# Performance work log

Hardware: AMD Instinct MI355X
Metric: run time of the kernel (lower is better)

The kernel has to match this reference:

```python
import jax, jax.numpy as jnp
import numpy as np

B, N, X, Y, W1, W2, D = 2, 6, 8, 8, 8, 8, 128
H, DH = 4, 32
L = X * Y          # number of windows
QT = N * W1 * W2   # tokens per window
EPS = 1e-5


def _ln(x, g, b):
    m = x.mean(-1, keepdims=True)
    v = ((x - m) ** 2).mean(-1, keepdims=True)
    return (x - m) * jax.lax.rsqrt(v + EPS) * g + b


def _win(t):
    # b n x y w1 w2 d -> b (x y) (n w1 w2) d
    return t.transpose(0, 2, 3, 1, 4, 5, 6).reshape(B, L, QT, D)


def setup_inputs() -> dict:
    key = jax.random.key(0)
    ks = jax.random.split(key, 12)
    s = 0.02
    inp = {
        'q': jax.random.normal(ks[0], (B, N, X, Y, W1, W2, D), jnp.float32),
        'k': jax.random.normal(ks[1], (B, N, X, Y, W1, W2, D), jnp.float32),
        'v': jax.random.normal(ks[2], (B, N, X, Y, W1, W2, D), jnp.float32),
        'skip': jax.random.normal(ks[3], (B, X, Y, W1, W2, D), jnp.float32),
        'gq': jnp.ones((D,), jnp.float32), 'betq': jnp.zeros((D,), jnp.float32),
        'gk': jnp.ones((D,), jnp.float32), 'betk': jnp.zeros((D,), jnp.float32),
        'gv': jnp.ones((D,), jnp.float32), 'betv': jnp.zeros((D,), jnp.float32),
        'wq': jax.random.normal(ks[4], (D, H * DH), jnp.float32) * s,
        'bq': jnp.zeros((H * DH,), jnp.float32),
        'wk': jax.random.normal(ks[5], (D, H * DH), jnp.float32) * s,
        'bk': jnp.zeros((H * DH,), jnp.float32),
        'wv': jax.random.normal(ks[6], (D, H * DH), jnp.float32) * s,
        'bv': jnp.zeros((H * DH,), jnp.float32),
        'wp': jax.random.normal(ks[7], (H * DH, D), jnp.float32) * s,
        'bp': jnp.zeros((D,), jnp.float32),
    }
    return inp


def reference(q, k, v, skip, gq, betq, gk, betk, gv, betv,
              wq, bq, wk, bk, wv, bv, wp, bp):
    scale = DH ** -0.5
    qw, kw, vw = _win(q), _win(k), _win(v)
    # LayerNorm + Linear QKV, split heads: (b, l, T, h, dh)
    qh = (_ln(qw, gq, betq) @ wq + bq).reshape(B, L, QT, H, DH)
    kh = (_ln(kw, gk, betk) @ wk + bk).reshape(B, L, QT, H, DH)
    vh = (_ln(vw, gv, betv) @ wv + bv).reshape(B, L, QT, H, DH)
    dot = scale * jnp.einsum('blqhd,blkhd->bhlqk', qh, kh)
    att = jax.nn.softmax(dot, axis=-1)
    a = jnp.einsum('bhlqk,blkhd->blqhd', att, vh).reshape(B, L, QT, H * DH)
    # b (x y) (n w1 w2) d -> b n x y w1 w2 d
    a = a.reshape(B, X, Y, N, W1, W2, H * DH).transpose(0, 3, 1, 2, 4, 5, 6)
    z = a @ wp + bp
    z = z.mean(1)  # average over views
    return z + skip
```

## Files before the change

### kernel.cpp

```cpp
#include <hip/hip_runtime.h>


typedef unsigned short u16;
typedef __bf16 bf16x8 __attribute__((ext_vector_type(8)));
typedef __bf16 bf16x4 __attribute__((ext_vector_type(4)));
typedef float  f32x16 __attribute__((ext_vector_type(16)));
typedef unsigned short u16x8 __attribute__((ext_vector_type(8)));

union U8 { u16x8 u; bf16x8 b; };

#if __has_builtin(__builtin_amdgcn_exp2f)
#define EXP2(x) __builtin_amdgcn_exp2f(x)
#else
#define EXP2(x) exp2f(x)
#endif

__device__ __forceinline__ f32x16 mfma_bf16(bf16x8 a, bf16x8 b, f32x16 c){
  return __builtin_amdgcn_mfma_f32_32x32x16_bf16(a, b, c, 0, 0, 0);
}


__global__ __launch_bounds__(512) void k_prep(
    const float* __restrict__ wq, const float* __restrict__ bq,
    const float* __restrict__ gq, const float* __restrict__ betq,
    const float* __restrict__ wk, const float* __restrict__ bk,
    const float* __restrict__ gk, const float* __restrict__ betk,
    const float* __restrict__ wv, const float* __restrict__ bv,
    const float* __restrict__ gv, const float* __restrict__ betv,
    const float* __restrict__ wp,
    u16* __restrict__ wqT, u16* __restrict__ wkT, u16* __restrict__ wvT, u16* __restrict__ wpT,
    float* __restrict__ bq2, float* __restrict__ bk2, float* __restrict__ bv2,
    float* __restrict__ uq2, float* __restrict__ uk2, float* __restrict__ uv2)
{
  __shared__ float wls[128*129];
  __shared__ float gls[128], bls[128];
  __shared__ float redb[512], redu[512];
  const float ALPHA_Q = 0.17677669529663687f * 1.4426950408889634f;
  int wsel = blockIdx.x, tid = threadIdx.x;
  const float *w, *bb, *g, *bet; u16* wT; float *b2, *u2; float alpha;
  if (wsel == 0){ w=wq; bb=bq; g=gq; bet=betq; wT=wqT; b2=bq2; u2=uq2; alpha=ALPHA_Q; }
  else if (wsel == 1){ w=wk; bb=bk; g=gk; bet=betk; wT=wkT; b2=bk2; u2=uk2; alpha=1.f; }
  else if (wsel == 2){ w=wv; bb=bv; g=gv; bet=betv; wT=wvT; b2=bv2; u2=uv2; alpha=1.f; }
  else { w=wp; bb=nullptr; g=nullptr; bet=nullptr; wT=wpT; b2=nullptr; u2=nullptr; alpha=1.f; }

  if (tid < 128){
    gls[tid] = g ? g[tid] : 1.f;
    bls[tid] = bet ? bet[tid] : 0.f;
  }
  const float4* w4 = (const float4*)w;
  #pragma unroll
  for (int i = 0; i < 8; i++){
    int idx = tid + i*512;
    int row = idx >> 5, c4 = (idx & 31) * 4;
    float4 x = w4[idx];
    wls[row*129 + c4 + 0] = x.x;
    wls[row*129 + c4 + 1] = x.y;
    wls[row*129 + c4 + 2] = x.z;
    wls[row*129 + c4 + 3] = x.w;
  }
  __syncthreads();
  int n = tid >> 2, qp = tid & 3;
  float sb = 0.f, su = 0.f;
  alignas(16) __bf16 tmp[32];
  #pragma unroll
  for (int kk = 0; kk < 32; kk++){
    int k2 = qp*32 + kk;
    float wv_ = wls[k2*129 + n];
    float gv_ = gls[k2];
    sb += bls[k2] * wv_;
    su += gv_ * wv_;
    tmp[kk] = (__bf16)(wv_ * gv_ * alpha);
  }
  #pragma unroll
  for (int j = 0; j < 4; j++)
    *(bf16x8*)(wT + n*128 + qp*32 + j*8) = *(bf16x8*)&tmp[j*8];
  redb[tid] = sb; redu[tid] = su;
  __syncthreads();
  if (qp == 0 && bb){
    float s = bb[n] + redb[tid] + redb[tid+1] + redb[tid+2] + redb[tid+3];
    float u = redu[tid] + redu[tid+1] + redu[tid+2] + redu[tid+3];
    b2[n] = s * alpha;
    u2[n] = u * alpha;
  }
}

__global__ __launch_bounds__(256) void k_lnproj(
    const float* __restrict__ qg, const float* __restrict__ kg, const float* __restrict__ vg,
    const u16* __restrict__ wqT, const u16* __restrict__ wkT, const u16* __restrict__ wvT,
    const float* __restrict__ bq2, const float* __restrict__ bk2, const float* __restrict__ bv2,
    const float* __restrict__ uq2, const float* __restrict__ uk2, const float* __restrict__ uv2,
    u16* __restrict__ qh, u16* __restrict__ kh, u16* __restrict__ vh)
{
  __shared__ alignas(16) u16 Abf[64*136];
  __shared__ float s1s[64], s2s[64];
  int bid = blockIdx.x, tid = threadIdx.x;
  int which = bid % 3;
  int t = bid / 3;
  int n = t % 6, bl = t / 6;
  const float* src; const u16* wT; const float *b2, *u2; u16* dstb;
  if (which == 0){ src=qg; wT=wqT; b2=bq2; u2=uq2; dstb=qh; }
  else if (which == 1){ src=kg; wT=wkT; b2=bk2; u2=uk2; dstb=kh; }
  else { src=vg; wT=wvT; b2=bv2; u2=uv2; dstb=vh; }
  int b = bl >> 6, l = bl & 63;
  const float4* s4 = (const float4*)(src + (size_t)((b*6 + n)*64 + l)*64*128);
  int row = tid >> 2, j = tid & 3;
  float s1 = 0.f, s2 = 0.f;
  #pragma unroll
  for (int i = 0; i < 8; i++){
    float4 xv = s4[row*32 + i*4 + j];
    s1 += xv.x + xv.y + xv.z + xv.w;
    s2 += xv.x*xv.x + xv.y*xv.y + xv.z*xv.z + xv.w*xv.w;
    bf16x4 pk;
    pk[0] = (__bf16)xv.x; pk[1] = (__bf16)xv.y;
    pk[2] = (__bf16)xv.z; pk[3] = (__bf16)xv.w;
    *(bf16x4*)&Abf[row*136 + (i*4 + j)*4] = pk;
  }
  s1 += __shfl_xor(s1, 1, 64); s1 += __shfl_xor(s1, 2, 64);
  s2 += __shfl_xor(s2, 1, 64); s2 += __shfl_xor(s2, 2, 64);
  if (j == 0){
    float m = s1 * (1.f/128.f);
    float r = rsqrtf(s2 * (1.f/128.f) - m*m + 1e-5f);
    s1s[row] = r;
    s2s[row] = r * m;
  }
  __syncthreads();
  int wave = tid >> 6, lane = tid & 63, lm = lane & 31, lh = lane >> 5;
  bf16x8 bfr[8];
  const u16* wrow = wT + (32*wave + lm)*128 + lh*8;
  #pragma unroll
  for (int ks = 0; ks < 8; ks++) bfr[ks] = *(const bf16x8*)(wrow + ks*16);
  f32x16 acc0, acc1;
  #pragma unroll
  for (int r = 0; r < 16; r++){ acc0[r]=0.f; acc1[r]=0.f; }
  #pragma unroll
  for (int ks = 0; ks < 8; ks++){
    bf16x8 a0 = *(const bf16x8*)&Abf[lm*136       + ks*16 + lh*8];
    bf16x8 a1 = *(const bf16x8*)&Abf[(32+lm)*136  + ks*16 + lh*8];
    acc0 = mfma_bf16(a0, bfr[ks], acc0);
    acc1 = mfma_bf16(a1, bfr[ks], acc1);
  }
  int col = 32*wave + lm;
  float u2c = u2[col], bc = b2[col];
  u16* dst = dstb + ((size_t)(bl*4 + wave)*384 + n*64)*32 + lm;
  #pragma unroll
  for (int r = 0; r < 16; r++){
    int row0 = (r&3) + 8*(r>>2) + 4*lh;
    float y0 = s1s[row0]     * acc0[r] - s2s[row0]     * u2c + bc;
    float y1 = s1s[row0+32]  * acc1[r] - s2s[row0+32]  * u2c + bc;
    *(__bf16*)&dst[(size_t)row0*32]      = (__bf16)y0;
    *(__bf16*)&dst[(size_t)(32+row0)*32] = (__bf16)y1;
  }
}

__global__ __launch_bounds__(768, 6) void k_attn(
    const u16* __restrict__ qh, const u16* __restrict__ kh, const u16* __restrict__ vh,
    u16* __restrict__ abar)
{
  __shared__ alignas(16) u16 vts[32*408];
  __shared__ float abar_s[64*32];
  int bid = blockIdx.x, tid = threadIdx.x;
  int h = bid & 3, bl = bid >> 2;
  const u16* qb = qh + (size_t)bid * (384*32);
  const u16* kb = kh + (size_t)bid * (384*32);
  const u16* vb = vh + (size_t)bid * (384*32);

  int wave = tid >> 6, lane = tid & 63, lm = lane & 31, lh = lane >> 5;
  int n = wave >> 1, qoff = (wave & 1) * 32;
  int qrow = n*64 + qoff + lm;

  bf16x8 qf0 = *(const bf16x8*)(qb + qrow*32 +      lh*8);
  bf16x8 qf1 = *(const bf16x8*)(qb + qrow*32 + 16 + lh*8);
  bf16x8 kf0[2], kf1[2];
  kf0[0] = *(const bf16x8*)(kb + lm*32 +      lh*8);
  kf1[0] = *(const bf16x8*)(kb + lm*32 + 16 + lh*8);

  #pragma unroll
  for (int i = 0; i < 2; i++){
    int c = tid + i*768;
    int key = c >> 2, part = c & 3;
    int u = key & 31, tt = key >> 5;
    int a = u >> 2;
    int anew = (a & 4) | ((a & 1) << 1) | ((a >> 1) & 1);
    int pos = tt*32 + anew*4 + (u & 3);
    u16x8 vv = *(const u16x8*)(vb + key*32 + part*8);
    #pragma unroll
    for (int jj = 0; jj < 8; jj++) vts[(part*8 + jj)*408 + pos] = vv[jj];
  }
  for (int idx = tid; idx < 2048; idx += 768) abar_s[idx] = 0.f;
  __syncthreads();

  const u16* vrow = &vts[lm*408 + 8*lh];
  U8 v0[2], v1[2];
  v0[0].u = *(const u16x8*)(vrow);
  v1[0].u = *(const u16x8*)(vrow + 16);

  f32x16 oacc;
  #pragma unroll
  for (int r = 0; r < 16; r++) oacc[r] = 0.f;
  float sle = 0.f;

  #pragma unroll
  for (int kt = 0; kt < 12; kt++){
    int cur = kt & 1, nxt = cur ^ 1;
    if (kt < 11){
      int K1 = (kt+1)*32;
      kf0[nxt] = *(const bf16x8*)(kb + (K1+lm)*32 +      lh*8);
      kf1[nxt] = *(const bf16x8*)(kb + (K1+lm)*32 + 16 + lh*8);
      v0[nxt].u = *(const u16x8*)(vrow + K1);
      v1[nxt].u = *(const u16x8*)(vrow + K1 + 16);
    }
    f32x16 s;
    #pragma unroll
    for (int r = 0; r < 16; r++) s[r] = 0.f;
    s = mfma_bf16(kf0[cur], qf0, s);
    s = mfma_bf16(kf1[cur], qf1, s);
    U8 p0, p1;
    #pragma unroll
    for (int r = 0; r < 8; r++){
      float e0 = EXP2(s[r]);
      float e1 = EXP2(s[r+8]);
      sle += e0 + e1;
      p0.b[r] = (__bf16)e0;
      p1.b[r] = (__bf16)e1;
    }
    oacc = mfma_bf16(p0.b, v0[cur].b, oacc);
    oacc = mfma_bf16(p1.b, v1[cur].b, oacc);
  }

  sle += __shfl_xor(sle, 32, 64);
  float inv = (1.f/6.f) / sle;

  #pragma unroll
  for (int r = 0; r < 16; r++){
    int q_l = (r&3) + 8*(r>>2) + 4*lh;
    float o = oacc[r] * __shfl(inv, q_l, 64);
    atomicAdd(&abar_s[(qoff + q_l)*32 + lm], o);
  }
  __syncthreads();
  u16* ob = abar + (size_t)(bl*64)*128 + h*32;
  for (int idx = tid; idx < 2048; idx += 768){
    int w12 = idx >> 5, dh = idx & 31;
    *(__bf16*)&ob[(size_t)w12*128 + dh] = (__bf16)abar_s[idx];
  }
}

__global__ __launch_bounds__(256) void k_out(
    const u16* __restrict__ abar, const u16* __restrict__ wpT,
    const float* __restrict__ bp, const float* __restrict__ skip,
    float* __restrict__ out)
{
  __shared__ alignas(16) u16 Als[64*136];
  int tid = threadIdx.x;
  int R0 = blockIdx.x * 64;
  #pragma unroll
  for (int i = 0; i < 4; i++){
    int c = tid + i*256;
    int row = c >> 4, part = c & 15;
    *(u16x8*)&Als[row*136 + part*8] = *(const u16x8*)(abar + (size_t)(R0+row)*128 + part*8);
  }
  __syncthreads();
  int wave = tid >> 6, lane = tid & 63, lm = lane & 31, lh = lane >> 5;
  bf16x8 bfr[8];
  const u16* wrow = wpT + (32*wave + lm)*128 + lh*8;
  #pragma unroll
  for (int ks = 0; ks < 8; ks++) bfr[ks] = *(const bf16x8*)(wrow + ks*16);
  f32x16 acc0, acc1;
  #pragma unroll
  for (int r = 0; r < 16; r++){ acc0[r]=0.f; acc1[r]=0.f; }
  #pragma unroll
  for (int ks = 0; ks < 8; ks++){
    bf16x8 a0 = *(const bf16x8*)&Als[lm*136      + ks*16 + lh*8];
    bf16x8 a1 = *(const bf16x8*)&Als[(32+lm)*136 + ks*16 + lh*8];
    acc0 = mfma_bf16(a0, bfr[ks], acc0);
    acc1 = mfma_bf16(a1, bfr[ks], acc1);
  }
  float bias = bp[32*wave + lm];
  #pragma unroll
  for (int r = 0; r < 16; r++){
    int row0 = (r&3) + 8*(r>>2) + 4*lh;
    size_t f0 = (size_t)(R0 + row0)*128 + 32*wave + lm;
    out[f0] = acc0[r] + bias + skip[f0];
    size_t f1 = (size_t)(R0 + 32 + row0)*128 + 32*wave + lm;
    out[f1] = acc1[r] + bias + skip[f1];
  }
}

extern "C" void kernel_launch(void* const* d_in, const int* in_sizes, int n_in,
                              void* d_out, int out_size, void* d_ws, size_t ws_size,
                              hipStream_t stream)
{
  const float* q    = (const float*)d_in[0];
  const float* k    = (const float*)d_in[1];
  const float* v    = (const float*)d_in[2];
  const float* skip = (const float*)d_in[3];
  const float* gq   = (const float*)d_in[4];
  const float* betq = (const float*)d_in[5];
  const float* gk   = (const float*)d_in[6];
  const float* betk = (const float*)d_in[7];
  const float* gv   = (const float*)d_in[8];
  const float* betv = (const float*)d_in[9];
  const float* wq   = (const float*)d_in[10];
  const float* bq   = (const float*)d_in[11];
  const float* wk   = (const float*)d_in[12];
  const float* bk   = (const float*)d_in[13];
  const float* wv   = (const float*)d_in[14];
  const float* bv   = (const float*)d_in[15];
  const float* wp   = (const float*)d_in[16];
  const float* bp   = (const float*)d_in[17];
  float* out = (float*)d_out;

  char* ws = (char*)d_ws;
  u16* wqT = (u16*)ws;
  u16* wkT = wqT + 16384;
  u16* wvT = wkT + 16384;
  u16* wpT = wvT + 16384;
  float* bq2 = (float*)(ws + 131072);
  float* bk2 = bq2 + 128;
  float* bv2 = bk2 + 128;
  float* uq2 = bv2 + 128;
  float* uk2 = uq2 + 128;
  float* uv2 = uk2 + 128;
  u16* qh = (u16*)(ws + 134144);
  u16* kh = qh + 6291456;
  u16* vh = kh + 6291456;
  u16* abar = vh + 6291456;

  k_prep  <<<4,    512, 0, stream>>>(wq,bq,gq,betq, wk,bk,gk,betk, wv,bv,gv,betv, wp,
                                     wqT,wkT,wvT,wpT, bq2,bk2,bv2, uq2,uk2,uv2);
  k_lnproj<<<2304, 256, 0, stream>>>(q,k,v, wqT,wkT,wvT, bq2,bk2,bv2, uq2,uk2,uv2, qh,kh,vh);
  k_attn  <<<512,  768, 0, stream>>>(qh,kh,vh, abar);
  k_out   <<<128,  256, 0, stream>>>(abar, wpT, bp, skip, out);
}
```

Measured before the change: 221.3 us.

## Stage K tile in padded LDS and split QK MFMA chains

Each attention block now cooperatively copies its whole K tile for one head into LDS, with rows padded to 36 elements, and reads K fragments from LDS instead of issuing per-wave global loads every iteration. The two QK MFMAs accumulate into separate registers and are summed before exp2, which breaks the dependency between them. Register double-buffering of the K and V fragments is removed, so V is now read from LDS inside each iteration. LDS use per block grows by about 27 KB, which may lower occupancy, and dropping the prefetch can expose LDS latency.

```diff
diff --git a/kernel.cpp b/kernel.cpp
--- a/kernel.cpp
+++ b/kernel.cpp
@@ -6,8 +6,9 @@
 typedef __bf16 bf16x4 __attribute__((ext_vector_type(4)));
 typedef float  f32x16 __attribute__((ext_vector_type(16)));
 typedef unsigned short u16x8 __attribute__((ext_vector_type(8)));
-
-union U8 { u16x8 u; bf16x8 b; };
+typedef unsigned short u16x4 __attribute__((ext_vector_type(4)));
+
+union U8 { u16x8 u; bf16x8 b; u16x4 h[2]; };
 
 #if __has_builtin(__builtin_amdgcn_exp2f)
 #define EXP2(x) __builtin_amdgcn_exp2f(x)
@@ -156,6 +157,7 @@
     const u16* __restrict__ qh, const u16* __restrict__ kh, const u16* __restrict__ vh,
     u16* __restrict__ abar)
 {
+  __shared__ alignas(16) u16 kls[384*36];
   __shared__ alignas(16) u16 vts[32*408];
   __shared__ float abar_s[64*32];
   int bid = blockIdx.x, tid = threadIdx.x;
@@ -170,10 +172,15 @@
 
   bf16x8 qf0 = *(const bf16x8*)(qb + qrow*32 +      lh*8);
   bf16x8 qf1 = *(const bf16x8*)(qb + qrow*32 + 16 + lh*8);
-  bf16x8 kf0[2], kf1[2];
-  kf0[0] = *(const bf16x8*)(kb + lm*32 +      lh*8);
-  kf1[0] = *(const bf16x8*)(kb + lm*32 + 16 + lh*8);
-
+
+  #pragma unroll
+  for (int i = 0; i < 2; i++){
+    int c = tid + i*768;
+    int key = c >> 2, part = c & 3;
+    U8 kv; kv.u = *(const u16x8*)(kb + key*32 + part*8);
+    *(u16x4*)&kls[key*36 + part*8]     = kv.h[0];
+    *(u16x4*)&kls[key*36 + part*8 + 4] = kv.h[1];
+  }
   #pragma unroll
   for (int i = 0; i < 2; i++){
     int c = tid + i*768;
@@ -190,9 +197,7 @@
   __syncthreads();
 
   const u16* vrow = &vts[lm*408 + 8*lh];
-  U8 v0[2], v1[2];
-  v0[0].u = *(const u16x8*)(vrow);
-  v1[0].u = *(const u16x8*)(vrow + 16);
+  const u16* krow = &kls[lm*36 + 8*lh];
 
   f32x16 oacc;
   #pragma unroll
@@ -201,30 +206,31 @@
 
   #pragma unroll
   for (int kt = 0; kt < 12; kt++){
-    int cur = kt & 1, nxt = cur ^ 1;
-    if (kt < 11){
-      int K1 = (kt+1)*32;
-      kf0[nxt] = *(const bf16x8*)(kb + (K1+lm)*32 +      lh*8);
-      kf1[nxt] = *(const bf16x8*)(kb + (K1+lm)*32 + 16 + lh*8);
-      v0[nxt].u = *(const u16x8*)(vrow + K1);
-      v1[nxt].u = *(const u16x8*)(vrow + K1 + 16);
-    }
-    f32x16 s;
+    const u16* kr = krow + kt*(32*36);
+    U8 kf0, kf1;
+    kf0.h[0] = *(const u16x4*)(kr);
+    kf0.h[1] = *(const u16x4*)(kr + 4);
+    kf1.h[0] = *(const u16x4*)(kr + 16);
+    kf1.h[1] = *(const u16x4*)(kr + 20);
+    f32x16 sa, sb_;
     #pragma unroll
-    for (int r = 0; r < 16; r++) s[r] = 0.f;
-    s = mfma_bf16(kf0[cur], qf0, s);
-    s = mfma_bf16(kf1[cur], qf1, s);
+    for (int r = 0; r < 16; r++){ sa[r] = 0.f; sb_[r] = 0.f; }
+    sa  = mfma_bf16(kf0.b, qf0, sa);
+    sb_ = mfma_bf16(kf1.b, qf1, sb_);
     U8 p0, p1;
     #pragma unroll
     for (int r = 0; r < 8; r++){
-      float e0 = EXP2(s[r]);
-      float e1 = EXP2(s[r+8]);
+      float e0 = EXP2(sa[r]   + sb_[r]);
+      float e1 = EXP2(sa[r+8] + sb_[r+8]);
       sle += e0 + e1;
       p0.b[r] = (__bf16)e0;
       p1.b[r] = (__bf16)e1;
     }
-    oacc = mfma_bf16(p0.b, v0[cur].b, oacc);
-    oacc = mfma_bf16(p1.b, v1[cur].b, oacc);
+    U8 v0, v1;
+    v0.u = *(const u16x8*)(vrow + kt*32);
+    v1.u = *(const u16x8*)(vrow + kt*32 + 16);
+    oacc = mfma_bf16(p0.b, v0.b, oacc);
+    oacc = mfma_bf16(p1.b, v1.b, oacc);
   }
 
   sle += __shfl_xor(sle, 32, 64);
```

After: 213.2 us. 3.7% less time.
